# Performance work log

Hardware: AMD Instinct MI355X
Metric: run time of the kernel (lower is better)

The kernel has to match this reference:

```python
import jax, jax.numpy as jnp
from jax import lax
import numpy as np

N, BITS, NCLS = 2048, 64, 100
LAMBDA = 1.0
ALPHA = 1.0


def setup_inputs() -> dict:
    key = jax.random.key(0)
    ku, kl = jax.random.split(key)
    u = jax.random.normal(ku, (N, BITS), dtype=jnp.float32)
    labels = jax.random.randint(kl, (N,), 0, NCLS)
    y = jax.nn.one_hot(labels, NCLS, dtype=jnp.float32)  # [N, C]
    return {"u": u, "y": y}


def reference(u, y):
    # inner_product[i, j] = <u_i, u_j>;  s[i, j] = (y_i . y_j > 0)
    ip = u @ u.T                      # [N, N]
    s = (y @ y.T) > 0                 # [N, N] bool

    def step(carry, xs):
        tot, cnt = carry
        ip_row, s_row = xs            # [N], [N]
        pos = s_row
        neg = ~s_row
        # triple[p, n] = ip[p] - ip[n] - ALPHA, clamped like the original
        T = jnp.clip(ip_row[:, None] - ip_row[None, :] - ALPHA, -100.0, 50.0)
        # -(T - log(1 + exp(T))) = softplus(T) - T
        L = jax.nn.softplus(T) - T    # [N, N]
        pm = (pos[:, None] & neg[None, :]).astype(L.dtype)
        npairs = pm.sum()
        valid = (pos.sum() > 0) & (neg.sum() > 0)
        row_loss = jnp.where(valid, (L * pm).sum() / jnp.maximum(npairs, 1.0), 0.0)
        return (tot + row_loss, cnt + valid.astype(jnp.float32)), None

    (tot, cnt), _ = lax.scan(step, (jnp.float32(0.0), jnp.float32(0.0)), (ip, s))
    loss1 = jnp.where(cnt > 0, tot / jnp.maximum(cnt, 1.0), 0.0)
    loss2 = LAMBDA * jnp.mean((u - jnp.sign(u)) ** 2)
    return loss1 + loss2
```

## Files before the change

### kernel.cpp

```cpp
#include <hip/hip_runtime.h>
#include <hip/hip_bf16.h>
#include <math.h>

#define NROWS 2048
#define BITS  64
#define NCLS  100
#define ALPHA_C  1.0f
#define LAMBDA_C 1.0f
#define ECLAMP   1.0e9f
#define NPMAX    64
#define EPS      20

typedef __bf16 bf16x8 __attribute__((ext_vector_type(8)));
typedef float  floatx4 __attribute__((ext_vector_type(4)));


__device__ __forceinline__ float block_reduce_sum(float v, float* wsum) {
    __syncthreads();
    #pragma unroll
    for (int off = 32; off > 0; off >>= 1) v += __shfl_down(v, off);
    int tid = threadIdx.x;
    if ((tid & 63) == 0) wsum[tid >> 6] = v;
    __syncthreads();
    float r = 0.f;
    if (tid == 0) {
        #pragma unroll
        for (int w = 0; w < 4; ++w) r += wsum[w];
    }
    return r;
}

__device__ __forceinline__ float softplus_mt(float T) {
    return fmaxf(-T, 0.f) + __logf(1.f + __expf(-fabsf(T)));
}


__global__ __launch_bounds__(256) void prep_kernel(const float* __restrict__ u,
                                                   const float* __restrict__ y,
                                                   unsigned short* __restrict__ ub,
                                                   unsigned char* __restrict__ lab8,
                                                   float* __restrict__ qp,
                                                   float* __restrict__ rl,
                                                   unsigned int* __restrict__ done) {
    const int tid = threadIdx.x;
    if (blockIdx.x < 64) {
        __shared__ float wsum[4];
        const int base = blockIdx.x * 2048 + tid * 8;
        float4 v0 = *(const float4*)(u + base);
        float4 v1 = *(const float4*)(u + base + 4);
        float vv[8] = {v0.x, v0.y, v0.z, v0.w, v1.x, v1.y, v1.z, v1.w};
        unsigned short ob[8];
        float q = 0.f;
        #pragma unroll
        for (int m = 0; m < 8; ++m) {
            const float v = vv[m];
            const float sg = (v > 0.f) ? 1.f : ((v < 0.f) ? -1.f : 0.f);
            const float d = v - sg;
            q = fmaf(d, d, q);
            __hip_bfloat16 h = __float2bfloat16(v);
            ob[m] = *reinterpret_cast<unsigned short*>(&h);
        }
        *(uint4*)(ub + base) = *(const uint4*)ob;
        float t = block_reduce_sum(q, wsum);
        if (tid == 0) qp[blockIdx.x] = t;
    } else {
        const int bi = blockIdx.x - 64;
        if (bi == 0 && tid == 0) *done = 0u;
        if (tid == 0) ((float4*)rl)[bi] = make_float4(0.f, 0.f, 0.f, 0.f);
        const int row = bi * 4 + (tid >> 6);
        const int lane = tid & 63;
        const float* yr = y + (size_t)row * NCLS;
        float v0 = yr[lane];
        float v1 = (lane < NCLS - 64) ? yr[lane + 64] : 0.f;
        unsigned long long m0 = __ballot(v0 > 0.5f);
        unsigned long long m1 = __ballot(v1 > 0.5f);
        if (lane == 0) {
            int c = m0 ? (__ffsll(m0) - 1) : (m1 ? 64 + __ffsll(m1) - 1 : 0);
            lab8[row] = (unsigned char)c;
        }
    }
}

__global__ __launch_bounds__(512, 4) void fused_kernel(const float* __restrict__ u,
                                                       const unsigned short* __restrict__ ub,
                                                       const unsigned char* __restrict__ lab8,
                                                       const float* __restrict__ qp,
                                                       float* __restrict__ rl,
                                                       unsigned int* __restrict__ done,
                                                       float* __restrict__ out) {
    __shared__ unsigned char labL[NROWS];
    __shared__ float uloc[16][BITS];
    __shared__ float epT[NPMAX][EPS];
    __shared__ int   clsIdx[NROWS];
    __shared__ int   ccnt[NCLS];
    __shared__ int   cofs[NCLS];
    __shared__ int   cpos[NCLS];
    __shared__ int   np16[16];
    __shared__ float wsum[16][8];
    __shared__ float red8[8];
    __shared__ int   lastflag;

    const int tid  = threadIdx.x;
    const int wave = tid >> 6;
    const int lane = tid & 63;
    const int rsel = lane & 15;
    const int quad = lane >> 4;
    const int koff = quad * 8;
    const int i0    = (blockIdx.x >> 2) * 16;
    const int jbase = (blockIdx.x & 3) * 512;

    ((unsigned int*)labL)[tid] = ((const unsigned int*)lab8)[tid];
    ((float2*)uloc)[tid] = ((const float2*)(u + (size_t)i0 * BITS))[tid];
    if (tid < NCLS) ccnt[tid] = 0;

    uint4 a0r = *(const uint4*)(ub + (size_t)(i0 + rsel) * BITS + koff);
    uint4 a1r = *(const uint4*)(ub + (size_t)(i0 + rsel) * BITS + 32 + koff);
    __syncthreads();

    #pragma unroll
    for (int m = 0; m < 4; ++m) atomicAdd(&ccnt[labL[tid + m * 512]], 1);
    __syncthreads();
    if (tid == 0) {
        int run = 0;
        for (int c = 0; c < NCLS; ++c) { cofs[c] = run; cpos[c] = run; run += ccnt[c]; }
    }
    __syncthreads();
    #pragma unroll
    for (int m = 0; m < 4; ++m) {
        const int j = tid + m * 512;
        const int p = atomicAdd(&cpos[labL[j]], 1);
        clsIdx[p] = j;
    }
    __syncthreads();

    #pragma unroll
    for (int s2 = 0; s2 < 2; ++s2) {
        const int r16 = wave * 2 + s2;
        const int ci  = labL[i0 + r16];
        const int np  = ccnt[ci];
        const int base = cofs[ci];
        const int npc = (np < NPMAX) ? np : NPMAX;
        float val = 0.f;
        if (lane < npc) {
            const int j = clsIdx[base + lane];
            const float4* uj4 = (const float4*)(u + (size_t)j * BITS);
            const float4* ui4 = (const float4*)(&uloc[r16][0]);
            float s0 = 0.f, s1 = 0.f, s2v = 0.f, s3 = 0.f;
            #pragma unroll
            for (int kk = 0; kk < BITS / 4; ++kk) {
                float4 vj = uj4[kk];
                float4 vi = ui4[kk];
                s0 = fmaf(vj.x, vi.x, s0);
                s1 = fmaf(vj.y, vi.y, s1);
                s2v = fmaf(vj.z, vi.z, s2v);
                s3 = fmaf(vj.w, vi.w, s3);
            }
            val = fminf(__expf(-((s0 + s1) + (s2v + s3))), ECLAMP);
        }
        epT[lane][r16] = val;
        if (lane == 0) np16[r16] = np;
    }
    __syncthreads();

    const bf16x8 A0 = __builtin_bit_cast(bf16x8, a0r);
    const bf16x8 A1 = __builtin_bit_cast(bf16x8, a1r);
    float Eb[4][4];
    #pragma unroll
    for (int t = 0; t < 4; ++t) {
        const int jr = jbase + (wave * 4 + t) * 16 + rsel;
        uint4 b0r = *(const uint4*)(ub + (size_t)jr * BITS + koff);
        uint4 b1r = *(const uint4*)(ub + (size_t)jr * BITS + 32 + koff);
        bf16x8 B0 = __builtin_bit_cast(bf16x8, b0r);
        bf16x8 B1 = __builtin_bit_cast(bf16x8, b1r);
        floatx4 cacc = {0.f, 0.f, 0.f, 0.f};
        cacc = __builtin_amdgcn_mfma_f32_16x16x32_bf16(A0, B0, cacc, 0, 0, 0);
        cacc = __builtin_amdgcn_mfma_f32_16x16x32_bf16(A1, B1, cacc, 0, 0, 0);
        const int colLab = labL[jr];
        #pragma unroll
        for (int r = 0; r < 4; ++r) {
            const int rowLab = labL[i0 + 4 * quad + r];
            Eb[t][r] = (colLab == rowLab) ? 0.f
                                          : fminf(__expf(cacc[r] + ALPHA_C), ECLAMP);
        }
    }

    int npmx = 0;
    #pragma unroll
    for (int r = 0; r < 16; ++r) {
        int n = np16[r]; n = (n > NPMAX) ? NPMAX : n;
        npmx = (n > npmx) ? n : npmx;
    }
    const int npr4 = (npmx + 3) & ~3;

    const float SC = 0x1p-60f;
    float mprod[4] = {1.f, 1.f, 1.f, 1.f};
    int   eacc[4]  = {0, 0, 0, 0};
    for (int k = 0; k < npr4; k += 4) {
        const float4 e0 = *(const float4*)(&epT[k][4 * quad]);
        const float4 e1 = *(const float4*)(&epT[k + 1][4 * quad]);
        const float4 e2 = *(const float4*)(&epT[k + 2][4 * quad]);
        const float4 e3 = *(const float4*)(&epT[k + 3][4 * quad]);
        const float e0c[4] = {e0.x * SC, e0.y * SC, e0.z * SC, e0.w * SC};
        const float e1v[4] = {e1.x, e1.y, e1.z, e1.w};
        const float e2c[4] = {e2.x * SC, e2.y * SC, e2.z * SC, e2.w * SC};
        const float e3v[4] = {e3.x, e3.y, e3.z, e3.w};
        #pragma unroll
        for (int t = 0; t < 4; ++t) {
            #pragma unroll
            for (int r = 0; r < 4; ++r) {
                const float q0 = Eb[t][r];
                const float f0 = fmaf(q0, e0c[r], SC);
                const float f1 = fmaf(q0, e1v[r], 1.f);
                const float f2 = fmaf(q0, e2c[r], SC);
                const float f3 = fmaf(q0, e3v[r], 1.f);
                const float P  = (f0 * f1) * (f2 * f3);
                const unsigned int pb = __builtin_bit_cast(unsigned int, P);
                eacc[r] += (int)(pb >> 23);
                const float m = __builtin_bit_cast(float,
                                    (pb & 0x007FFFFFu) | 0x3F800000u);
                mprod[r] *= m;
            }
        }
    }
    const float nadj = 7.0f * (float)npr4;
    float s[4];
    #pragma unroll
    for (int r = 0; r < 4; ++r)
        s[r] = ((float)eacc[r] - nadj) + __log2f(mprod[r]);

    #pragma unroll
    for (int r = 0; r < 4; ++r) {
        #pragma unroll
        for (int off = 1; off < 16; off <<= 1) s[r] += __shfl_xor(s[r], off);
    }
    if (rsel == 0) {
        #pragma unroll
        for (int r = 0; r < 4; ++r) wsum[4 * quad + r][wave] = s[r];
    }
    __syncthreads();
    if (tid < 16) {
        const float ln2 = 0.6931471805599453f;
        const float tot = (((wsum[tid][0] + wsum[tid][1]) +
                            (wsum[tid][2] + wsum[tid][3])) +
                           ((wsum[tid][4] + wsum[tid][5]) +
                            (wsum[tid][6] + wsum[tid][7]))) * ln2;
        atomicAdd(&rl[i0 + tid], tot);
    }
    __syncthreads();

    if (tid == 0) {
        __threadfence();
        const unsigned int old = atomicAdd(done, 1u);
        lastflag = (old == 511u) ? 1 : 0;
    }
    __syncthreads();
    if (lastflag) {
        float tsum = 0.f, vsum = 0.f;
        for (int row = tid; row < NROWS; row += 512) {
            const float rv = atomicAdd(&rl[row], 0.0f);
            const int np = ccnt[labL[row]];
            const int nn = NROWS - np;
            const int valid = (np > 0 && nn > 0) ? 1 : 0;
            tsum += valid ? (rv / fmaxf((float)np * (float)nn, 1.f)) : 0.f;
            vsum += (float)valid;
        }
        float q = (tid < 64) ? qp[tid] : 0.f;

        float vals[3] = {tsum, vsum, q};
        float outv[3];
        #pragma unroll
        for (int m = 0; m < 3; ++m) {
            float v = vals[m];
            #pragma unroll
            for (int off = 32; off > 0; off >>= 1) v += __shfl_down(v, off);
            if (lane == 0) red8[wave] = v;
            __syncthreads();
            float r = 0.f;
            if (tid == 0) {
                #pragma unroll
                for (int w = 0; w < 8; ++w) r += red8[w];
            }
            __syncthreads();
            outv[m] = r;
        }
        if (tid == 0) {
            const float loss1 = (outv[1] > 0.f) ? (outv[0] / fmaxf(outv[1], 1.f)) : 0.f;
            const float loss2 = LAMBDA_C * (outv[2] / (float)(NROWS * BITS));
            out[0] = loss1 + loss2;
        }
    }
}


__global__ __launch_bounds__(256) void labels_only_kernel(const float* __restrict__ y,
                                                          int* __restrict__ labels) {
    const int tid = threadIdx.x;
    const int row = blockIdx.x * 4 + (tid >> 6);
    const int lane = tid & 63;
    const float* yr = y + (size_t)row * NCLS;
    float v0 = yr[lane];
    float v1 = (lane < NCLS - 64) ? yr[lane + 64] : 0.f;
    unsigned long long m0 = __ballot(v0 > 0.5f);
    unsigned long long m1 = __ballot(v1 > 0.5f);
    if (lane == 0) {
        int c = m0 ? (__ffsll(m0) - 1) : (m1 ? 64 + __ffsll(m1) - 1 : 0);
        labels[row] = c;
    }
}

__global__ __launch_bounds__(256) void row_loss_kernel(const float* __restrict__ u,
                                                       const int* __restrict__ labels,
                                                       float* __restrict__ acc) {
    __shared__ float a[NROWS];
    __shared__ float apv[NROWS];
    __shared__ int lab[NROWS];
    __shared__ float ui[BITS];
    __shared__ int npos_s;
    __shared__ float wsum[4];

    const int i = blockIdx.x;
    const int tid = threadIdx.x;

    if (tid < BITS) ui[tid] = u[(size_t)i * BITS + tid];
    if (tid == 0) npos_s = 0;
    __syncthreads();

    #pragma unroll
    for (int m = 0; m < NROWS / 256; ++m) {
        const int j = tid + m * 256;
        const float4* uj = (const float4*)(u + (size_t)j * BITS);
        float s0 = 0.f, s1 = 0.f, s2 = 0.f, s3 = 0.f;
        #pragma unroll
        for (int q = 0; q < BITS / 4; ++q) {
            float4 v = uj[q];
            s0 = fmaf(v.x, ui[4 * q + 0], s0);
            s1 = fmaf(v.y, ui[4 * q + 1], s1);
            s2 = fmaf(v.z, ui[4 * q + 2], s2);
            s3 = fmaf(v.w, ui[4 * q + 3], s3);
        }
        a[j] = (s0 + s1) + (s2 + s3);
        lab[j] = labels[j];
    }
    __syncthreads();

    const int c = lab[i];
    #pragma unroll
    for (int m = 0; m < NROWS / 256; ++m) {
        const int j = tid + m * 256;
        if (lab[j] == c) { int k = atomicAdd(&npos_s, 1); apv[k] = a[j]; }
    }
    __syncthreads();
    const int npos = npos_s;
    const int nneg = NROWS - npos;

    float b[NROWS / 256];
    #pragma unroll
    for (int m = 0; m < NROWS / 256; ++m) {
        const int j = tid + m * 256;
        b[m] = (lab[j] != c) ? (a[j] + ALPHA_C) : -3.0e38f;
    }

    float lsum = 0.f;
    for (int k = 0; k < npos; ++k) {
        const float apk = apv[k];
        #pragma unroll
        for (int m = 0; m < NROWS / 256; ++m) lsum += softplus_mt(apk - b[m]);
    }

    float tot = block_reduce_sum(lsum, wsum);
    if (tid == 0) {
        const int valid = (npos > 0 && nneg > 0) ? 1 : 0;
        const float npairs = fmaxf((float)npos * (float)nneg, 1.f);
        const float rlv = valid ? (tot / npairs) : 0.f;
        atomicAdd(&acc[0], rlv);
        atomicAdd(&acc[1], (float)valid);
    }
}

__global__ __launch_bounds__(256) void quant_kernel(const float* __restrict__ u,
                                                    float* __restrict__ acc) {
    __shared__ float wsum[4];
    const int stride = gridDim.x * 256;
    float s = 0.f;
    for (int t = blockIdx.x * 256 + threadIdx.x; t < NROWS * BITS; t += stride) {
        float v = u[t];
        float sg = (v > 0.f) ? 1.f : ((v < 0.f) ? -1.f : 0.f);
        float d = v - sg;
        s = fmaf(d, d, s);
    }
    float tot = block_reduce_sum(s, wsum);
    if (threadIdx.x == 0) atomicAdd(&acc[2], tot);
}

__global__ void finalize_kernel(const float* __restrict__ acc,
                                float* __restrict__ out) {
    const float tot = acc[0], cnt = acc[1], q = acc[2];
    const float loss1 = (cnt > 0.f) ? (tot / fmaxf(cnt, 1.f)) : 0.f;
    const float loss2 = LAMBDA_C * (q / (float)(NROWS * BITS));
    out[0] = loss1 + loss2;
}


extern "C" void kernel_launch(void* const* d_in, const int* in_sizes, int n_in,
                              void* d_out, int out_size, void* d_ws, size_t ws_size,
                              hipStream_t stream) {
    const float* u = (const float*)d_in[0];
    const float* y = (const float*)d_in[1];
    float* out = (float*)d_out;

    unsigned char* lab8 = (unsigned char*)d_ws;
    unsigned int* done = (unsigned int*)((char*)d_ws + 4096);
    float* rl = (float*)((char*)d_ws + 8192);
    float* qp = (float*)((char*)d_ws + 16384);
    unsigned short* ub = (unsigned short*)((char*)d_ws + 24576);
    const size_t NEED = 24576 + (size_t)NROWS * BITS * sizeof(unsigned short);

    if (ws_size >= NEED) {
        prep_kernel<<<576, 256, 0, stream>>>(u, y, ub, lab8, qp, rl, done);
        fused_kernel<<<512, 512, 0, stream>>>(u, ub, lab8, qp, rl, done, out);
    } else {
        float* acc2 = (float*)d_ws;
        int*   lab2 = (int*)((char*)d_ws + 256);
        hipMemsetAsync(d_ws, 0, 256, stream);
        labels_only_kernel<<<512, 256, 0, stream>>>(y, lab2);
        row_loss_kernel<<<NROWS, 256, 0, stream>>>(u, lab2, acc2);
        quant_kernel<<<64, 256, 0, stream>>>(u, acc2);
        finalize_kernel<<<1, 1, 0, stream>>>(acc2, out);
    }
}
```

Before: 81.98 us.

## Process rows in class-sorted order and build class index with ballot ranking

Replaces the shared-memory atomic counting sort with a ballot-based per-wave ranking, chunk histograms and a shuffle prefix scan to build the class-sorted index. Each block now takes 16 rows in class-sorted order, so the rows in a block share few classes. This makes the per-block max positive count (npmx) tighter and cuts the inner product loop length. The MFMA stage also moves ahead of a barrier to overlap with the epT writes. The cost is more setup code and indirect row gathers for u and ub.

```diff
diff --git a/kernel.cpp b/kernel.cpp
--- a/kernel.cpp
+++ b/kernel.cpp
@@ -10,6 +10,7 @@
 #define ECLAMP   1.0e9f
 #define NPMAX    64
 #define EPS      20
+#define NCHUNK   32
 
 typedef __bf16 bf16x8 __attribute__((ext_vector_type(8)));
 typedef float  floatx4 __attribute__((ext_vector_type(4)));
@@ -92,9 +93,9 @@
     __shared__ float uloc[16][BITS];
     __shared__ float epT[NPMAX][EPS];
     __shared__ int   clsIdx[NROWS];
+    __shared__ int   whist[NCHUNK][NCLS];
     __shared__ int   ccnt[NCLS];
     __shared__ int   cofs[NCLS];
-    __shared__ int   cpos[NCLS];
     __shared__ int   np16[16];
     __shared__ float wsum[16][8];
     __shared__ float red8[8];
@@ -110,33 +111,83 @@
     const int jbase = (blockIdx.x & 3) * 512;
 
     ((unsigned int*)labL)[tid] = ((const unsigned int*)lab8)[tid];
-    ((float2*)uloc)[tid] = ((const float2*)(u + (size_t)i0 * BITS))[tid];
-    if (tid < NCLS) ccnt[tid] = 0;
-
-    uint4 a0r = *(const uint4*)(ub + (size_t)(i0 + rsel) * BITS + koff);
-    uint4 a1r = *(const uint4*)(ub + (size_t)(i0 + rsel) * BITS + 32 + koff);
-    __syncthreads();
-
-    #pragma unroll
-    for (int m = 0; m < 4; ++m) atomicAdd(&ccnt[labL[tid + m * 512]], 1);
-    __syncthreads();
-    if (tid == 0) {
+    {
+        int* wf = &whist[0][0];
+        #pragma unroll
+        for (int k = 0; k < 7; ++k) {
+            const int idx = tid + k * 512;
+            if (idx < NCHUNK * NCLS) wf[idx] = 0;
+        }
+    }
+    __syncthreads();
+
+    int rk[4], rc[4];
+    const unsigned long long below = (1ull << lane) - 1ull;
+    #pragma unroll
+    for (int s = 0; s < 4; ++s) {
+        const int t = wave * 4 + s;
+        const int c = labL[t * 64 + lane];
+        unsigned long long m = ~0ull;
+        #pragma unroll
+        for (int b = 0; b < 7; ++b) {
+            const unsigned long long bb = __ballot((c >> b) & 1);
+            m &= ((c >> b) & 1) ? bb : ~bb;
+        }
+        rk[s] = (int)__popcll(m & below);
+        rc[s] = c;
+        whist[t][c] = (int)__popcll(m);
+    }
+    __syncthreads();
+
+    if (tid < NCLS) {
         int run = 0;
-        for (int c = 0; c < NCLS; ++c) { cofs[c] = run; cpos[c] = run; run += ccnt[c]; }
-    }
-    __syncthreads();
-    #pragma unroll
-    for (int m = 0; m < 4; ++m) {
-        const int j = tid + m * 512;
-        const int p = atomicAdd(&cpos[labL[j]], 1);
-        clsIdx[p] = j;
-    }
-    __syncthreads();
+        #pragma unroll
+        for (int t = 0; t < NCHUNK; ++t) {
+            const int v = whist[t][tid];
+            whist[t][tid] = run;
+            run += v;
+        }
+        ccnt[tid] = run;
+    }
+    __syncthreads();
+
+    if (tid < 64) {
+        const int c0 = (tid < 50) ? ccnt[2 * tid] : 0;
+        const int c1 = (tid < 50) ? ccnt[2 * tid + 1] : 0;
+        int p = c0 + c1;
+        #pragma unroll
+        for (int off = 1; off < 64; off <<= 1) {
+            const int n = __shfl_up(p, off);
+            if (tid >= off) p += n;
+        }
+        const int excl = p - (c0 + c1);
+        if (tid < 50) { cofs[2 * tid] = excl; cofs[2 * tid + 1] = excl + c0; }
+    }
+    __syncthreads();
+
+    #pragma unroll
+    for (int s = 0; s < 4; ++s) {
+        const int t = wave * 4 + s;
+        const int c = rc[s];
+        clsIdx[cofs[c] + whist[t][c] + rk[s]] = t * 64 + lane;
+    }
+    __syncthreads();
+
+    {
+        const int gr = tid >> 5;
+        const int gp = tid & 31;
+        const int grow = clsIdx[i0 + gr];
+        ((float2*)&uloc[gr][0])[gp] =
+            ((const float2*)(u + (size_t)grow * BITS))[gp];
+    }
+    const int arow = clsIdx[i0 + rsel];
+    uint4 a0r = *(const uint4*)(ub + (size_t)arow * BITS + koff);
+    uint4 a1r = *(const uint4*)(ub + (size_t)arow * BITS + 32 + koff);
 
     #pragma unroll
     for (int s2 = 0; s2 < 2; ++s2) {
         const int r16 = wave * 2 + s2;
-        const int ci  = labL[i0 + r16];
+        const int ci  = labL[clsIdx[i0 + r16]];
         const int np  = ccnt[ci];
         const int base = cofs[ci];
         const int npc = (np < NPMAX) ? np : NPMAX;
@@ -160,7 +211,10 @@
         epT[lane][r16] = val;
         if (lane == 0) np16[r16] = np;
     }
-    __syncthreads();
+
+    int rlabq[4];
+    #pragma unroll
+    for (int r = 0; r < 4; ++r) rlabq[r] = labL[clsIdx[i0 + 4 * quad + r]];
 
     const bf16x8 A0 = __builtin_bit_cast(bf16x8, a0r);
     const bf16x8 A1 = __builtin_bit_cast(bf16x8, a1r);
@@ -178,11 +232,11 @@
         const int colLab = labL[jr];
         #pragma unroll
         for (int r = 0; r < 4; ++r) {
-            const int rowLab = labL[i0 + 4 * quad + r];
-            Eb[t][r] = (colLab == rowLab) ? 0.f
-                                          : fminf(__expf(cacc[r] + ALPHA_C), ECLAMP);
-        }
-    }
+            Eb[t][r] = (colLab == rlabq[r]) ? 0.f
+                                            : fminf(__expf(cacc[r] + ALPHA_C), ECLAMP);
+        }
+    }
+    __syncthreads();
 
     int npmx = 0;
     #pragma unroll
@@ -244,7 +298,7 @@
                             (wsum[tid][2] + wsum[tid][3])) +
                            ((wsum[tid][4] + wsum[tid][5]) +
                             (wsum[tid][6] + wsum[tid][7]))) * ln2;
-        atomicAdd(&rl[i0 + tid], tot);
+        atomicAdd(&rl[clsIdx[i0 + tid]], tot);
     }
     __syncthreads();
 
```

Measured after the change: 82.67 us. Within noise of the previous version (+0.8%).
